# Kernel optimization log

Measured on AMD Instinct MI355X. Metric: run time of the kernel, lower is better.

Reference implementation:

```python
import jax, jax.numpy as jnp
import numpy as np

GRID_SIZE = 5
SPLINE_ORDER = 3
B, D, O = 16384, 512, 512


def _make_grid():
    h = 2.0 / GRID_SIZE
    # matches torch.arange(-k, grid_size + k + 1) * h - 2.0  -> 12 knots
    return jnp.arange(-SPLINE_ORDER, GRID_SIZE + SPLINE_ORDER + 1, dtype=jnp.float32) * h - 2.0


def _bspline_basis(x, grid):
    # x: [B, D]; grid: [G] with G = grid_size + 2*order + 1 = 12
    G = grid.shape[0]
    xe = x[..., None]                      # [B, D, 1]
    g = grid.reshape(1, 1, G)              # [1, 1, G]
    # degree-0: indicator of knot interval  -> [B, D, G-1]
    bases = ((xe >= g[:, :, :-1]) & (xe < g[:, :, 1:])).astype(x.dtype)
    eps = 1e-9
    for k in range(1, SPLINE_ORDER + 1):   # Cox-de Boor recursion, width shrinks by 1 each step
        left = (xe - g[:, :, :-k - 1]) / (g[:, :, k:-1] - g[:, :, :-k - 1] + eps)
        right = (g[:, :, k + 1:] - xe) / (g[:, :, k + 1:] - g[:, :, 1:-k] + eps)
        bases = left * bases[..., :-1] + right * bases[..., 1:]
    return bases                           # [B, D, grid_size + order] = [B, D, 8]


def setup_inputs() -> dict:
    key = jax.random.key(0)
    k1, k2, k3 = jax.random.split(key, 3)
    x = jax.random.normal(k1, (B, D), dtype=jnp.float32)
    # kaiming_uniform_(a=sqrt(5)*0.1): bound = sqrt(6 / ((1 + a^2) * fan_in))
    a = np.sqrt(5.0) * 0.1
    bound = float(np.sqrt(6.0 / ((1.0 + a * a) * D)))
    base_weight = jax.random.uniform(k2, (O, D), dtype=jnp.float32, minval=-bound, maxval=bound)
    spline_weight = jax.random.normal(k3, (O, D, GRID_SIZE + SPLINE_ORDER), dtype=jnp.float32) * 0.01
    return {"x": x, "base_weight": base_weight, "spline_weight": spline_weight}


def reference(x, base_weight, spline_weight):
    grid = _make_grid()
    base_output = jnp.matmul(jax.nn.silu(x), base_weight.T)      # [B, O]
    x_norm = jnp.clip(x, -2.0, 2.0)
    basis = _bspline_basis(x_norm, grid)                          # [B, D, 8]
    spline_output = jnp.einsum('bic,oic->bo', basis, spline_weight)
    return base_output + spline_output
```

## Files before the change

### kernel.cpp

```cpp
#include <hip/hip_runtime.h>
#include <cstdint>
#include <cstddef>
#include <type_traits>

#define B_ROWS 16384
#define D_DIM  512
#define O_DIM  512
#define BM 128
#define BN 256
#define BK 32

typedef __bf16 bf16;
typedef __attribute__((ext_vector_type(8))) bf16  bf16x8;
typedef __attribute__((ext_vector_type(4))) float f32x4;

__device__ __forceinline__ uint32_t pk2(float a, float b) {
    uint16_t ua = __builtin_bit_cast(uint16_t, (__bf16)a);
    uint16_t ub = __builtin_bit_cast(uint16_t, (__bf16)b);
    return (uint32_t)ua | ((uint32_t)ub << 16);
}

__device__ __forceinline__ void spline_pairs(float xv, uint32_t out[4]) {
    float xn = fminf(fmaxf(xv, -2.0f), 2.0f);
    float t  = (xn + 3.2f) * 2.5f;
    int   j0 = (int)t;
    float u  = t - (float)j0;
    float u2 = u * u, u3 = u2 * u, omu = 1.0f - u;
    const float s6 = 1.0f / 6.0f;
    float w0 = omu * omu * omu * s6;
    float w1 = (3.0f * u3 - 6.0f * u2 + 4.0f) * s6;
    float w2 = (-3.0f * u3 + 3.0f * u2 + 3.0f * u + 1.0f) * s6;
    float w3 = u3 * s6;
    uint64_t W64 = ((uint64_t)pk2(w2, w3) << 32) | pk2(w0, w1);
    int sh = (j0 - 3) * 16;
    uint64_t lo = W64 << (sh & 63);
    uint64_t hi = W64 >> ((64 - sh) & 63);
    uint32_t lo_lo = (uint32_t)lo, lo_hi = (uint32_t)(lo >> 32);
    uint32_t hi_lo = (uint32_t)hi, hi_hi = (uint32_t)(hi >> 32);
    bool lt64 = sh < 64, eq0 = (sh == 0), lt128 = sh < 128;
    out[0] = lt64 ? lo_lo : 0u;
    out[1] = lt64 ? lo_hi : 0u;
    out[2] = lt64 ? (eq0 ? 0u : hi_lo) : (lt128 ? lo_lo : 0u);
    out[3] = lt64 ? (eq0 ? 0u : hi_hi) : (lt128 ? lo_hi : 0u);
}

__global__ void pack_w_kernel(const float* __restrict__ bw,
                              const float* __restrict__ sw,
                              bf16* __restrict__ W) {
    int idx = blockIdx.x * blockDim.x + threadIdx.x;
    if (idx >= O_DIM * 64) return;
    int o  = idx >> 6;
    int i0 = (idx & 63) * 8;

    bf16 ob[9][8];
    const float* bwp = bw + (size_t)o * D_DIM + i0;
#pragma unroll
    for (int e = 0; e < 8; e++) {
        ob[0][e] = (bf16)bwp[e];
        const float* sp = sw + ((size_t)o * D_DIM + i0 + e) * 8;
#pragma unroll
        for (int c = 0; c < 8; c++)
            ob[c + 1][e] = (bf16)sp[c];
    }
    const int c   = i0 >> 5;
    const int sub = (i0 & 31) >> 3;
    const int cb  = o >> 4;
    const int ln  = (o & 15) + sub * 16;
#pragma unroll
    for (int f = 0; f < 9; f++) {
        size_t off = ((size_t)((f * 16 + c) * 32 + cb) * 64 + ln) * 8;
        *(bf16x8*)(W + off) = *(const bf16x8*)ob[f];
    }
}

#define BARA asm volatile("s_waitcnt lgkmcnt(0)\n\ts_barrier" ::: "memory")

__global__ __launch_bounds__(512, 2)
void gemm_fused_kernel(const float* __restrict__ x, const bf16* __restrict__ Wf,
                       float* __restrict__ C) {
    __shared__ __align__(16) bf16 As0[BM * BK], As1[BM * BK], As2[BM * BK], As3[BM * BK];

    const int tid  = threadIdx.x;
    const int bid  = blockIdx.x;
    const int n0   = (bid & 1) * BN;
    const int m0   = (bid >> 1) * BM;
    const int wave = tid >> 6;
    const int lane = tid & 63;
    const int wm   = (wave >> 2) * 64;
    const int wn   = (wave & 3) * 64;
    const int l15  = lane & 15;
    const int quad = lane >> 4;
    const int swz  = (l15 >> 1) & 3;
    const int aoff = l15 * BK + (quad ^ swz) * 8;

    const int rA = tid >> 2;
    const int q8 = tid & 3;
    const float* xrow = x + (size_t)(m0 + rA) * D_DIM + q8 * 8;
    const int awo = rA * BK + ((q8 ^ ((rA >> 1) & 3)) * 8);

    const bf16* gBf = Wf + ((size_t)(((n0 + wn) >> 4) * 64 + lane)) * 8;

    bf16* const AsArr[4] = {As0, As1, As2, As3};

    f32x4 acc[4][4] = {};
    bf16x8 brA[4], brB[4];
    uint32_t vpk[2][4][8];
    float xe[8];

    auto write_pack = [&](bf16* slab, const uint32_t (&P)[4][8], int j) {
        const int pr = j >> 1;
        uint32_t o[4];
#pragma unroll
        for (int m = 0; m < 4; m++) {
            uint32_t lo = P[pr][2*m], hi = P[pr][2*m+1];
            o[m] = (j & 1) ? ((lo >> 16) | (hi & 0xFFFF0000u))
                           : ((lo & 0xFFFFu) | (hi << 16));
        }
        *(uint4*)(slab + awo) = *(const uint4*)o;
    };
    auto write_silu = [&](bf16* slab) {
        float sl[8];
#pragma unroll
        for (int e = 0; e < 8; e++)
            sl[e] = xe[e] * __builtin_amdgcn_rcpf(1.0f + __expf(-xe[e]));
        uint32_t o[4] = {pk2(sl[0],sl[1]), pk2(sl[2],sl[3]),
                         pk2(sl[4],sl[5]), pk2(sl[6],sl[7])};
        *(uint4*)(slab + awo) = *(const uint4*)o;
    };

    {
#pragma unroll
        for (int jn = 0; jn < 4; jn++)
            brA[jn] = *(const bf16x8*)(gBf + jn * 512);
        float4 a = *(const float4*)xrow;
        float4 b = *(const float4*)(xrow + 4);
        xe[0]=a.x; xe[1]=a.y; xe[2]=a.z; xe[3]=a.w;
        xe[4]=b.x; xe[5]=b.y; xe[6]=b.z; xe[7]=b.w;
#pragma unroll
        for (int e = 0; e < 8; e++) {
            uint32_t o4[4];
            spline_pairs(xe[e], o4);
            vpk[0][0][e]=o4[0]; vpk[0][1][e]=o4[1];
            vpk[0][2][e]=o4[2]; vpk[0][3][e]=o4[3];
        }
        write_silu(As0);
        write_pack(As1, vpk[0], 0);
        BARA;
    }

    auto step_body = [&](auto c4v, auto fv, int c) {
        constexpr int C4 = decltype(c4v)::value;
        constexpr int F  = decltype(fv)::value;
        constexpr int PC = C4 & 1;
        constexpr int TP = (C4 + F) & 1;
        constexpr int AR = (C4 + F) & 3;
        constexpr int AW = (C4 + F + 2) & 3;

        if (F == 0 && c < 15) {
            float4 a = *(const float4*)(xrow + (c + 1) * 32);
            float4 b = *(const float4*)(xrow + (c + 1) * 32 + 4);
            xe[0]=a.x; xe[1]=a.y; xe[2]=a.z; xe[3]=a.w;
            xe[4]=b.x; xe[5]=b.y; xe[6]=b.z; xe[7]=b.w;
        }
        if (!(c == 15 && F == 8)) {
            const int tN = (F < 8) ? ((F + 1) * 16 + c) : (c + 1);
            const bf16* src = gBf + (size_t)tN * 16384;
            if constexpr (TP == 0) {
#pragma unroll
                for (int jn = 0; jn < 4; jn++)
                    brB[jn] = *(const bf16x8*)(src + jn * 512);
            } else {
#pragma unroll
                for (int jn = 0; jn < 4; jn++)
                    brA[jn] = *(const bf16x8*)(src + jn * 512);
            }
        }
        bf16x8 af[4];
#pragma unroll
        for (int tt = 0; tt < 4; tt++)
            af[tt] = *(const bf16x8*)(AsArr[AR] + (wm + tt * 16) * BK + aoff);

        if (F >= 1 && c < 15) {
            uint32_t o4[4];
            spline_pairs(xe[F - 1], o4);
            vpk[PC ^ 1][0][F-1]=o4[0]; vpk[PC ^ 1][1][F-1]=o4[1];
            vpk[PC ^ 1][2][F-1]=o4[2]; vpk[PC ^ 1][3][F-1]=o4[3];
        }
        if constexpr (F <= 6) {
            write_pack(AsArr[AW], vpk[PC], F + 1);
        } else if constexpr (F == 7) {
            if (c < 15) write_silu(AsArr[AW]);
        } else {
            if (c < 15) write_pack(AsArr[AW], vpk[PC ^ 1], 0);
        }

        __builtin_amdgcn_s_setprio(1);
#pragma unroll
        for (int im = 0; im < 4; im++)
#pragma unroll
            for (int jn = 0; jn < 4; jn++)
                acc[im][jn] = __builtin_amdgcn_mfma_f32_16x16x32_bf16(
                    af[im], (TP == 0) ? brA[jn] : brB[jn], acc[im][jn], 0, 0, 0);
        __builtin_amdgcn_s_setprio(0);

        if constexpr (TP == 1) {
            if (!(c == 15 && F == 8)) BARA;
        }
    };

#define IC(n) std::integral_constant<int,(n)>{}
    auto chunk_body = [&](auto c4v, int c) {
        step_body(c4v, IC(0), c); step_body(c4v, IC(1), c); step_body(c4v, IC(2), c);
        step_body(c4v, IC(3), c); step_body(c4v, IC(4), c); step_body(c4v, IC(5), c);
        step_body(c4v, IC(6), c); step_body(c4v, IC(7), c); step_body(c4v, IC(8), c);
    };

    for (int cc = 0; cc < 16; cc += 4) {
        chunk_body(IC(0), cc);
        chunk_body(IC(1), cc + 1);
        chunk_body(IC(2), cc + 2);
        chunk_body(IC(3), cc + 3);
    }
#undef IC

#pragma unroll
    for (int im = 0; im < 4; im++) {
        const int rbase = m0 + wm + im * 16 + quad * 4;
#pragma unroll
        for (int jn = 0; jn < 4; jn++) {
            const int col = n0 + wn + jn * 16 + l15;
#pragma unroll
            for (int rr = 0; rr < 4; rr++)
                C[(size_t)(rbase + rr) * O_DIM + col] = acc[im][jn][rr];
        }
    }
}

extern "C" void kernel_launch(void* const* d_in, const int* in_sizes, int n_in,
                              void* d_out, int out_size, void* d_ws, size_t ws_size,
                              hipStream_t stream) {
    const float* x  = (const float*)d_in[0];
    const float* bw = (const float*)d_in[1];
    const float* sw = (const float*)d_in[2];
    float* out = (float*)d_out;

    const size_t Wbytes = (size_t)144 * 32 * 64 * 8 * sizeof(bf16);
    if (ws_size < Wbytes) return;
    bf16* W = (bf16*)d_ws;

    pack_w_kernel<<<(O_DIM * 64 + 255) / 256, 256, 0, stream>>>(bw, sw, W);
    gemm_fused_kernel<<<dim3(B_ROWS / BM * (O_DIM / BN)), dim3(512), 0, stream>>>(x, W, out);
}
```

Baseline: 167.9 us.

## Retile GEMM to 64x512 blocks so each x row's spline basis is computed once

Changes the block tile from 128x256 to 64x512, so each block covers all output columns and the eight waves split only along N. Previously each x row's spline basis and SiLU were computed twice, once by each N-half block. Now each thread expands 4 x values instead of 8, which halves the redundant elementwise work. In exchange, B-operand loads per block double relative to MFMA work, since each wave now covers 64 rows instead of sharing reuse across a 128-row tile. The LDS A-tile writes also shrink to 8 bytes per thread.

```diff
diff --git a/kernel.cpp b/kernel.cpp
--- a/kernel.cpp
+++ b/kernel.cpp
@@ -6,8 +6,8 @@
 #define B_ROWS 16384
 #define D_DIM  512
 #define O_DIM  512
-#define BM 128
-#define BN 256
+#define BM 64
+#define BN 512
 #define BK 32
 
 typedef __bf16 bf16;
@@ -82,50 +82,47 @@
 
     const int tid  = threadIdx.x;
     const int bid  = blockIdx.x;
-    const int n0   = (bid & 1) * BN;
-    const int m0   = (bid >> 1) * BM;
+    const int m0   = bid * BM;
     const int wave = tid >> 6;
     const int lane = tid & 63;
-    const int wm   = (wave >> 2) * 64;
-    const int wn   = (wave & 3) * 64;
+    const int wn   = wave * 64;
     const int l15  = lane & 15;
     const int quad = lane >> 4;
     const int swz  = (l15 >> 1) & 3;
     const int aoff = l15 * BK + (quad ^ swz) * 8;
 
-    const int rA = tid >> 2;
-    const int q8 = tid & 3;
-    const float* xrow = x + (size_t)(m0 + rA) * D_DIM + q8 * 8;
-    const int awo = rA * BK + ((q8 ^ ((rA >> 1) & 3)) * 8);
-
-    const bf16* gBf = Wf + ((size_t)(((n0 + wn) >> 4) * 64 + lane)) * 8;
+    const int rA = tid >> 3;
+    const int q4 = tid & 7;
+    const float* xrow = x + (size_t)(m0 + rA) * D_DIM + q4 * 4;
+    const int awo = rA * BK + (((q4 >> 1) ^ ((rA >> 1) & 3)) * 8) + (q4 & 1) * 4;
+
+    const bf16* gBf = Wf + ((size_t)((wn >> 4) * 64 + lane)) * 8;
 
     bf16* const AsArr[4] = {As0, As1, As2, As3};
 
     f32x4 acc[4][4] = {};
     bf16x8 brA[4], brB[4];
-    uint32_t vpk[2][4][8];
-    float xe[8];
-
-    auto write_pack = [&](bf16* slab, const uint32_t (&P)[4][8], int j) {
+    uint32_t vpk[2][4][4];
+    float xe[4];
+
+    auto write_pack = [&](bf16* slab, const uint32_t (&P)[4][4], int j) {
         const int pr = j >> 1;
-        uint32_t o[4];
-#pragma unroll
-        for (int m = 0; m < 4; m++) {
+        uint32_t o[2];
+#pragma unroll
+        for (int m = 0; m < 2; m++) {
             uint32_t lo = P[pr][2*m], hi = P[pr][2*m+1];
             o[m] = (j & 1) ? ((lo >> 16) | (hi & 0xFFFF0000u))
                            : ((lo & 0xFFFFu) | (hi << 16));
         }
-        *(uint4*)(slab + awo) = *(const uint4*)o;
+        *(uint2*)(slab + awo) = *(const uint2*)o;
     };
     auto write_silu = [&](bf16* slab) {
-        float sl[8];
-#pragma unroll
-        for (int e = 0; e < 8; e++)
+        float sl[4];
+#pragma unroll
+        for (int e = 0; e < 4; e++)
             sl[e] = xe[e] * __builtin_amdgcn_rcpf(1.0f + __expf(-xe[e]));
-        uint32_t o[4] = {pk2(sl[0],sl[1]), pk2(sl[2],sl[3]),
-                         pk2(sl[4],sl[5]), pk2(sl[6],sl[7])};
-        *(uint4*)(slab + awo) = *(const uint4*)o;
+        uint32_t o[2] = {pk2(sl[0],sl[1]), pk2(sl[2],sl[3])};
+        *(uint2*)(slab + awo) = *(const uint2*)o;
     };
 
     {
@@ -133,11 +130,9 @@
         for (int jn = 0; jn < 4; jn++)
             brA[jn] = *(const bf16x8*)(gBf + jn * 512);
         float4 a = *(const float4*)xrow;
-        float4 b = *(const float4*)(xrow + 4);
         xe[0]=a.x; xe[1]=a.y; xe[2]=a.z; xe[3]=a.w;
-        xe[4]=b.x; xe[5]=b.y; xe[6]=b.z; xe[7]=b.w;
-#pragma unroll
-        for (int e = 0; e < 8; e++) {
+#pragma unroll
+        for (int e = 0; e < 4; e++) {
             uint32_t o4[4];
             spline_pairs(xe[e], o4);
             vpk[0][0][e]=o4[0]; vpk[0][1][e]=o4[1];
@@ -158,9 +153,7 @@
 
         if (F == 0 && c < 15) {
             float4 a = *(const float4*)(xrow + (c + 1) * 32);
-            float4 b = *(const float4*)(xrow + (c + 1) * 32 + 4);
             xe[0]=a.x; xe[1]=a.y; xe[2]=a.z; xe[3]=a.w;
-            xe[4]=b.x; xe[5]=b.y; xe[6]=b.z; xe[7]=b.w;
         }
         if (!(c == 15 && F == 8)) {
             const int tN = (F < 8) ? ((F + 1) * 16 + c) : (c + 1);
@@ -178,13 +171,15 @@
         bf16x8 af[4];
 #pragma unroll
         for (int tt = 0; tt < 4; tt++)
-            af[tt] = *(const bf16x8*)(AsArr[AR] + (wm + tt * 16) * BK + aoff);
-
-        if (F >= 1 && c < 15) {
-            uint32_t o4[4];
-            spline_pairs(xe[F - 1], o4);
-            vpk[PC ^ 1][0][F-1]=o4[0]; vpk[PC ^ 1][1][F-1]=o4[1];
-            vpk[PC ^ 1][2][F-1]=o4[2]; vpk[PC ^ 1][3][F-1]=o4[3];
+            af[tt] = *(const bf16x8*)(AsArr[AR] + tt * 16 * BK + aoff);
+
+        if constexpr (F >= 1 && F <= 4) {
+            if (c < 15) {
+                uint32_t o4[4];
+                spline_pairs(xe[F - 1], o4);
+                vpk[PC ^ 1][0][F-1]=o4[0]; vpk[PC ^ 1][1][F-1]=o4[1];
+                vpk[PC ^ 1][2][F-1]=o4[2]; vpk[PC ^ 1][3][F-1]=o4[3];
+            }
         }
         if constexpr (F <= 6) {
             write_pack(AsArr[AW], vpk[PC], F + 1);
@@ -225,10 +220,10 @@
 
 #pragma unroll
     for (int im = 0; im < 4; im++) {
-        const int rbase = m0 + wm + im * 16 + quad * 4;
+        const int rbase = m0 + im * 16 + quad * 4;
 #pragma unroll
         for (int jn = 0; jn < 4; jn++) {
-            const int col = n0 + wn + jn * 16 + l15;
+            const int col = wn + jn * 16 + l15;
 #pragma unroll
             for (int rr = 0; rr < 4; rr++)
                 C[(size_t)(rbase + rr) * O_DIM + col] = acc[im][jn][rr];
@@ -249,5 +244,5 @@
     bf16* W = (bf16*)d_ws;
 
     pack_w_kernel<<<(O_DIM * 64 + 255) / 256, 256, 0, stream>>>(bw, sw, W);
-    gemm_fused_kernel<<<dim3(B_ROWS / BM * (O_DIM / BN)), dim3(512), 0, stream>>>(x, W, out);
-}
+    gemm_fused_kernel<<<dim3(B_ROWS / BM), dim3(512), 0, stream>>>(x, W, out);
+}
```

Result: faster. 152.8 us (-9.0%).
